# Kernel optimization log

Hardware: AMD Instinct MI355X
Metric: run time of the kernel (lower is better)

Reference implementation:

```python
import jax, jax.numpy as jnp
import numpy as np

N_NODES = 50000
N_EDGES = 400000
D = 128


def _rgg_layer(x, src, tgt, Wk, Wq, Wv, Ws, b, n_nodes):
    # Node-level projections (dense GEMMs, as in PyG which applies Linear before message passing)
    k = x @ Wk  # lin_key, gathered at targets
    q = x @ Wq  # lin_query, gathered at sources
    v = x @ Wv  # lin_value, gathered at sources
    # Per-edge gather + sigmoid gate + elementwise message
    eta = jax.nn.sigmoid(k[tgt] + q[src])  # [E, D]
    msg = eta * v[src]                      # [E, D]
    # Scatter-add aggregation to target nodes
    agg = jax.ops.segment_sum(msg, tgt, num_segments=n_nodes)
    # Root/skip connection + bias
    return agg + x @ Ws + b


def setup_inputs() -> dict:
    key = jax.random.key(0)
    ks = jax.random.split(key, 12)
    s = 1.0 / np.sqrt(D)
    x = jax.random.normal(ks[0], (N_NODES, D), dtype=jnp.float32)
    edge_index = jax.random.randint(ks[1], (2, N_EDGES), 0, N_NODES, dtype=jnp.int64)
    W = lambda k: (jax.random.normal(k, (D, D), dtype=jnp.float32) * s)
    return {
        "x": x,
        "edge_index": edge_index,
        "Wk1": W(ks[2]), "Wq1": W(ks[3]), "Wv1": W(ks[4]), "Ws1": W(ks[5]),
        "b1": jnp.zeros((D,), dtype=jnp.float32),
        "Wk2": W(ks[6]), "Wq2": W(ks[7]), "Wv2": W(ks[8]), "Ws2": W(ks[9]),
        "b2": jnp.zeros((D,), dtype=jnp.float32),
    }


def reference(x, edge_index, Wk1, Wq1, Wv1, Ws1, b1, Wk2, Wq2, Wv2, Ws2, b2):
    src, tgt = edge_index[0], edge_index[1]
    n = x.shape[0]
    h = _rgg_layer(x, src, tgt, Wk1, Wq1, Wv1, Ws1, b1, n)
    h = jax.nn.relu(h)
    # F.dropout treated as identity (deterministic/inference reference)
    out = _rgg_layer(h, src, tgt, Wk2, Wq2, Wv2, Ws2, b2, n)
    return out
```

## Files before the change

kernel.cpp:

```cpp
#include <hip/hip_runtime.h>

#define N_NODES 50000
#define D 128
#define N_EDGES 400000
#define NCHUNKS ((N_NODES + 255) / 256)
#define NBLK32 ((N_NODES + 31) / 32)
#define W_FRAG_SHORTS 16384

#define MW_BLOCKS  64
#define HIST_BLOCKS ((N_EDGES + 255) / 256)
#define PREP_BLOCKS (MW_BLOCKS + HIST_BLOCKS)

typedef short s8v  __attribute__((ext_vector_type(8)));
typedef float f4v  __attribute__((ext_vector_type(4)));

__device__ __forceinline__ unsigned int f2bf(float f) {
    unsigned int u = __float_as_uint(f);
    u += 0x7FFFu + ((u >> 16) & 1u);
    return u >> 16;
}
__device__ __forceinline__ unsigned int packbf(float a, float b) {
    return (f2bf(b) << 16) | f2bf(a);
}
__device__ __forceinline__ float bflo(unsigned int u) { return __uint_as_float(u << 16); }
__device__ __forceinline__ float bfhi(unsigned int u) { return __uint_as_float(u & 0xFFFF0000u); }
__device__ __forceinline__ float sigm(float x) {
    return __builtin_amdgcn_rcpf(1.f + __expf(-x));
}

__global__ __launch_bounds__(256)
void prep_all(const float* __restrict__ W0, const float* __restrict__ W1,
              const float* __restrict__ W2, const float* __restrict__ W3,
              const float* __restrict__ W4, const float* __restrict__ W5,
              const float* __restrict__ W6, const float* __restrict__ W7,
              short* __restrict__ Wt,
              const int* __restrict__ tgt, int* __restrict__ counts)
{
    const int b = blockIdx.x;
    if (b < MW_BLOCKS) {
        const int wsel = b >> 3;
        const float* W = (wsel == 0) ? W0 : (wsel == 1) ? W1 : (wsel == 2) ? W2 :
                         (wsel == 3) ? W3 : (wsel == 4) ? W4 : (wsel == 5) ? W5 :
                         (wsel == 6) ? W6 : W7;
        const int slot = (b & 7) * 256 + threadIdx.x;
        const int frag = slot >> 6;
        const int lane = slot & 63;
        const int n    = (frag >> 2) * 16 + (lane & 15);
        const int kc   = frag & 3;
        const int quad = lane >> 4;
        const int k0   = kc * 32 + quad * 8;
        s8v v;
#pragma unroll
        for (int j = 0; j < 8; ++j)
            v[j] = (short)f2bf(W[(size_t)(k0 + j) * D + n]);
        *(s8v*)(Wt + (size_t)wsel * W_FRAG_SHORTS + (size_t)slot * 8) = v;
    } else {
        const int e = (b - MW_BLOCKS) * 256 + threadIdx.x;
        if (e < N_EDGES) atomicAdd(&counts[tgt[e]], 1);
    }
}

__global__ __launch_bounds__(256)
void csr_scan(const int* __restrict__ counts, int* __restrict__ off,
              int* __restrict__ cursor, int* __restrict__ done_ctr,
              int* __restrict__ chunk_sum)
{
    __shared__ int s[256];
    const int b = blockIdx.x, t = threadIdx.x;
    const int i = b * 256 + t;
    const int v = (i < N_NODES) ? counts[i] : 0;
    s[t] = v;
    __syncthreads();
    for (int d = 1; d < 256; d <<= 1) {
        int tt = (t >= d) ? s[t - d] : 0;
        __syncthreads();
        s[t] += tt;
        __syncthreads();
    }
    const int incl = s[t];

    if (t == 255) {
        __hip_atomic_store(&chunk_sum[b], incl, __ATOMIC_RELAXED, __HIP_MEMORY_SCOPE_AGENT);
        __hip_atomic_fetch_add(done_ctr, 1, __ATOMIC_RELEASE, __HIP_MEMORY_SCOPE_AGENT);
    }
    if (t == 0) {
        while (__hip_atomic_load(done_ctr, __ATOMIC_ACQUIRE, __HIP_MEMORY_SCOPE_AGENT) < NCHUNKS)
            __builtin_amdgcn_s_sleep(8);
    }
    __syncthreads();

    const int pv = (t < b) ? __hip_atomic_load(&chunk_sum[t], __ATOMIC_RELAXED,
                                               __HIP_MEMORY_SCOPE_AGENT) : 0;
    __syncthreads();
    s[t] = pv;
    __syncthreads();
    for (int d = 128; d > 0; d >>= 1) {
        if (t < d) s[t] += s[t + d];
        __syncthreads();
    }
    const int base = s[0];

    if (i < N_NODES) {
        const int excl = base + incl - v;
        off[i]    = excl;
        cursor[i] = excl;
    }
    if (b == 0 && t == 0) off[N_NODES] = N_EDGES;
}

__device__ __forceinline__
void mfma_phase32(const short* As, const short* __restrict__ Wf,
                  int lane, int w, f4v acc[2][2])
{
    s8v bv[2][4];
#pragma unroll
    for (int nt2 = 0; nt2 < 2; ++nt2)
#pragma unroll
        for (int kc = 0; kc < 4; ++kc)
            bv[nt2][kc] = *(const s8v*)(Wf + (((2 * w + nt2) * 4 + kc) * 64 + lane) * 8);
#pragma unroll
    for (int mt = 0; mt < 2; ++mt)
#pragma unroll
        for (int nt2 = 0; nt2 < 2; ++nt2)
            acc[mt][nt2] = (f4v){0.f, 0.f, 0.f, 0.f};
#pragma unroll
    for (int kc = 0; kc < 4; ++kc) {
        const int sl = (lane ^ (kc << 1)) * 8;
        s8v a0 = *(const s8v*)&As[(0 * 4 + kc) * 512 + sl];
        s8v a1 = *(const s8v*)&As[(1 * 4 + kc) * 512 + sl];
#pragma unroll
        for (int nt2 = 0; nt2 < 2; ++nt2) {
            acc[0][nt2] = __builtin_amdgcn_mfma_f32_16x16x32_bf16(a0, bv[nt2][kc], acc[0][nt2], 0, 0, 0);
            acc[1][nt2] = __builtin_amdgcn_mfma_f32_16x16x32_bf16(a1, bv[nt2][kc], acc[1][nt2], 0, 0, 0);
        }
    }
}

__device__ __forceinline__
void c_to_lds32(float* Cs, int lane, int w, const f4v acc[2][2])
{
#pragma unroll
    for (int mt = 0; mt < 2; ++mt) {
        const int r0 = mt * 16 + (lane >> 4) * 4;
#pragma unroll
        for (int nt2 = 0; nt2 < 2; ++nt2) {
            const int col = w * 32 + nt2 * 16 + (lane & 15);
            const int g = col >> 2, jj = col & 3;
#pragma unroll
            for (int i = 0; i < 4; ++i) {
                const int row = r0 + i;
                const int gs  = g ^ (((row >> 2) & 3) << 2);
                Cs[row * 128 + gs * 4 + jj] = acc[mt][nt2][i];
            }
        }
    }
}

template<bool X_FP32, bool AGG_BF16>
__device__ __forceinline__
void gemm_tile(int m0, const float* __restrict__ Xf, const short* __restrict__ Xb,
               const short* __restrict__ WtL, const float* __restrict__ bias,
               short* __restrict__ Kb, unsigned int* __restrict__ QV,
               float* __restrict__ AggF, unsigned int* __restrict__ AggB,
               short* As, float* Cs, float* biasS)
{
    const int tid  = threadIdx.x;
    const int lane = tid & 63;
    const int w    = tid >> 6;

    if (tid < 128) biasS[tid] = bias[tid];

#pragma unroll
    for (int i = 0; i < 2; ++i) {
        const int m   = (tid >> 4) + 16 * i;
        const int oct = tid & 15;
        const int row = m0 + m;
        s8v v = (s8v){0, 0, 0, 0, 0, 0, 0, 0};
        if (row < N_NODES) {
            if (X_FP32) {
                const float* p = Xf + (size_t)row * D + oct * 8;
                float4 a0 = *(const float4*)p;
                float4 a1 = *(const float4*)(p + 4);
                v[0] = (short)f2bf(a0.x); v[1] = (short)f2bf(a0.y);
                v[2] = (short)f2bf(a0.z); v[3] = (short)f2bf(a0.w);
                v[4] = (short)f2bf(a1.x); v[5] = (short)f2bf(a1.y);
                v[6] = (short)f2bf(a1.z); v[7] = (short)f2bf(a1.w);
            } else {
                v = *(const s8v*)(Xb + (size_t)row * D + oct * 8);
            }
        }
        const int kc = oct >> 2, quad = oct & 3;
        const int frag = (m >> 4) * 4 + kc;
        const int slot = ((m & 15) + 16 * quad) ^ (kc << 1);
        *(s8v*)&As[frag * 512 + slot * 8] = v;
    }

    f4v acc[2][2], accV[2][2];
    __syncthreads();

    mfma_phase32(As, WtL + 0 * W_FRAG_SHORTS, lane, w, acc);
    c_to_lds32(Cs, lane, w, acc);
    __syncthreads();
#pragma unroll
    for (int j = 0; j < 4; ++j) {
        const int c   = tid + 256 * j;
        const int row = c >> 5, gg = c & 31;
        const int gs  = gg ^ (((row >> 2) & 3) << 2);
        const f4v vv  = *(const f4v*)&Cs[row * 128 + gs * 4];
        const int grow = m0 + row;
        if (grow < N_NODES) {
            uint2* kp = (uint2*)((unsigned int*)Kb + (size_t)grow * 64 + gg * 2);
            *kp = make_uint2(packbf(vv[0], vv[1]), packbf(vv[2], vv[3]));
        }
    }
    __syncthreads();

    mfma_phase32(As, WtL + 1 * W_FRAG_SHORTS, lane, w, acc);
    mfma_phase32(As, WtL + 2 * W_FRAG_SHORTS, lane, w, accV);
    c_to_lds32(Cs, lane, w, acc);
    __syncthreads();
    unsigned int qp0[4], qp1[4];
#pragma unroll
    for (int j = 0; j < 4; ++j) {
        const int c   = tid + 256 * j;
        const int row = c >> 5, gg = c & 31;
        const int gs  = gg ^ (((row >> 2) & 3) << 2);
        const f4v vv  = *(const f4v*)&Cs[row * 128 + gs * 4];
        qp0[j] = packbf(vv[0], vv[1]);
        qp1[j] = packbf(vv[2], vv[3]);
    }
    __syncthreads();
    c_to_lds32(Cs, lane, w, accV);
    __syncthreads();
#pragma unroll
    for (int j = 0; j < 4; ++j) {
        const int c   = tid + 256 * j;
        const int row = c >> 5, gg = c & 31;
        const int gs  = gg ^ (((row >> 2) & 3) << 2);
        const f4v vv  = *(const f4v*)&Cs[row * 128 + gs * 4];
        const int grow = m0 + row;
        if (grow < N_NODES) {
            uint4* qvp = (uint4*)(QV + (size_t)grow * 128 + gg * 4);
            *qvp = make_uint4(qp0[j], packbf(vv[0], vv[1]),
                              qp1[j], packbf(vv[2], vv[3]));
        }
    }
    __syncthreads();

    mfma_phase32(As, WtL + 3 * W_FRAG_SHORTS, lane, w, acc);
    c_to_lds32(Cs, lane, w, acc);
    __syncthreads();
#pragma unroll
    for (int j = 0; j < 4; ++j) {
        const int c   = tid + 256 * j;
        const int row = c >> 5, gg = c & 31;
        const int gs  = gg ^ (((row >> 2) & 3) << 2);
        const f4v vv  = *(const f4v*)&Cs[row * 128 + gs * 4];
        const int grow = m0 + row;
        if (grow >= N_NODES) continue;
        const float4 bv = *(const float4*)&biasS[gg * 4];
        const float o0 = vv[0] + bv.x, o1 = vv[1] + bv.y;
        const float o2 = vv[2] + bv.z, o3 = vv[3] + bv.w;
        if (AGG_BF16) {
            uint2* ap = (uint2*)(AggB + (size_t)grow * 64 + gg * 2);
            *ap = make_uint2(packbf(o0, o1), packbf(o2, o3));
        } else {
            *(float4*)&AggF[(size_t)grow * D + gg * 4] = make_float4(o0, o1, o2, o3);
        }
    }
}

__global__ __launch_bounds__(256, 4)
void gemm1_scatter(const float* __restrict__ X, const short* __restrict__ WtL,
                   const float* __restrict__ bias,
                   short* __restrict__ Kb, unsigned int* __restrict__ QV,
                   unsigned int* __restrict__ AggB,
                   const int* __restrict__ src, const int* __restrict__ tgt,
                   int* __restrict__ cursor, int* __restrict__ es)
{
    __shared__ __align__(16) short As[4096];
    __shared__ __align__(16) float Cs[4096];
    __shared__ __align__(16) float biasS[128];

    if (blockIdx.x < NBLK32) {
        gemm_tile<true, true>(blockIdx.x * 32, X, nullptr, WtL, bias,
                              Kb, QV, nullptr, AggB, As, Cs, biasS);
    } else {
        const int e = (blockIdx.x - NBLK32) * 256 + threadIdx.x;
        if (e < N_EDGES) {
            int pos = atomicAdd(&cursor[tgt[e]], 1);
            es[pos] = src[e];
        }
    }
}

__global__ __launch_bounds__(256, 4)
void gemm2(const short* __restrict__ Hb, const short* __restrict__ WtL,
           const float* __restrict__ bias,
           short* __restrict__ Kb, unsigned int* __restrict__ QV,
           float* __restrict__ AggF)
{
    __shared__ __align__(16) short As[4096];
    __shared__ __align__(16) float Cs[4096];
    __shared__ __align__(16) float biasS[128];
    gemm_tile<false, false>(blockIdx.x * 32, nullptr, Hb, WtL, bias,
                            Kb, QV, AggF, nullptr, As, Cs, biasS);
}

template<bool FIRST>
__global__ __launch_bounds__(256)
void node_agg(const int* __restrict__ off, const int* __restrict__ es,
              const short* __restrict__ K, const unsigned int* __restrict__ QV,
              const void* __restrict__ Skip, float* __restrict__ OutF,
              unsigned int* __restrict__ Hb)
{
    const int lane = threadIdx.x & 63;
    const int t    = __builtin_amdgcn_readfirstlane(blockIdx.x * 4 + (threadIdx.x >> 6));

    const unsigned int ku = ((const unsigned int*)K)[(size_t)t * 64 + lane];
    const float kx = bflo(ku), ky = bfhi(ku);

    float skx, sky;
    if (FIRST) {
        const unsigned int su = ((const unsigned int*)Skip)[(size_t)t * 64 + lane];
        skx = bflo(su); sky = bfhi(su);
    } else {
        const float2 s2 = ((const float2*)Skip)[(size_t)t * 64 + lane];
        skx = s2.x; sky = s2.y;
    }

    float ax = 0.f, ay = 0.f, bx = 0.f, by = 0.f;
    const int e0 = __builtin_amdgcn_readfirstlane(off[t]);
    const int e1 = __builtin_amdgcn_readfirstlane(off[t + 1]);

    int e = e0;
    for (; e + 8 <= e1; e += 8) {
        const int sv = es[e + (lane & 7)];
        uint2 g[8];
#pragma unroll
        for (int u = 0; u < 8; ++u) {
            const int s = __builtin_amdgcn_readlane(sv, u);
            g[u] = ((const uint2*)(QV + (size_t)s * 128))[lane];
        }
#pragma unroll
        for (int u = 0; u < 8; ++u) {
            if (u & 1) {
                bx += bflo(g[u].y) * sigm(kx + bflo(g[u].x));
                by += bfhi(g[u].y) * sigm(ky + bfhi(g[u].x));
            } else {
                ax += bflo(g[u].y) * sigm(kx + bflo(g[u].x));
                ay += bfhi(g[u].y) * sigm(ky + bfhi(g[u].x));
            }
        }
    }
    if (e + 4 <= e1) {
        const int sv = es[e + (lane & 3)];
        uint2 g[4];
#pragma unroll
        for (int u = 0; u < 4; ++u) {
            const int s = __builtin_amdgcn_readlane(sv, u);
            g[u] = ((const uint2*)(QV + (size_t)s * 128))[lane];
        }
#pragma unroll
        for (int u = 0; u < 4; ++u) {
            if (u & 1) {
                bx += bflo(g[u].y) * sigm(kx + bflo(g[u].x));
                by += bfhi(g[u].y) * sigm(ky + bfhi(g[u].x));
            } else {
                ax += bflo(g[u].y) * sigm(kx + bflo(g[u].x));
                ay += bfhi(g[u].y) * sigm(ky + bfhi(g[u].x));
            }
        }
        e += 4;
    }
    for (; e < e1; ++e) {
        const int s0 = __builtin_amdgcn_readfirstlane(es[e]);
        const uint2 g0 = ((const uint2*)(QV + (size_t)s0 * 128))[lane];
        ax += bflo(g0.y) * sigm(kx + bflo(g0.x));
        ay += bfhi(g0.y) * sigm(ky + bfhi(g0.x));
    }

    const float rx = skx + ax + bx;
    const float ry = sky + ay + by;

    if (FIRST) {
        Hb[(size_t)t * 64 + lane] = packbf(fmaxf(rx, 0.f), fmaxf(ry, 0.f));
    } else {
        ((float2*)OutF)[(size_t)t * 64 + lane] = make_float2(rx, ry);
    }
}

extern "C" void kernel_launch(void* const* d_in, const int* in_sizes, int n_in,
                              void* d_out, int out_size, void* d_ws, size_t ws_size,
                              hipStream_t stream)
{
    const float* x   = (const float*)d_in[0];
    const int*   ei  = (const int*)d_in[1];
    const float* Wk1 = (const float*)d_in[2];
    const float* Wq1 = (const float*)d_in[3];
    const float* Wv1 = (const float*)d_in[4];
    const float* Ws1 = (const float*)d_in[5];
    const float* b1  = (const float*)d_in[6];
    const float* Wk2 = (const float*)d_in[7];
    const float* Wq2 = (const float*)d_in[8];
    const float* Wv2 = (const float*)d_in[9];
    const float* Ws2 = (const float*)d_in[10];
    const float* b2  = (const float*)d_in[11];

    const int* src = ei;
    const int* tgt = ei + N_EDGES;

    const size_t nd = (size_t)N_NODES * D;
    short* kb   = (short*)d_ws;
    short* qv   = kb + nd;
    short* hb   = qv + 2 * nd;
    short* ag1  = hb + nd;
    short* wt   = ag1 + nd;
    int* counts    = (int*)(wt + 8 * W_FRAG_SHORTS);
    int* done_ctr  = counts + N_NODES;
    int* off       = counts + N_NODES + 2;
    int* cursor    = off + N_NODES + 1;
    int* es        = cursor + N_NODES;
    int* chunk_sum = es + N_EDGES;
    float* out = (float*)d_out;

    hipMemsetAsync(counts, 0, (N_NODES + 2) * sizeof(int), stream);
    prep_all<<<PREP_BLOCKS, 256, 0, stream>>>(Wk1, Wq1, Wv1, Ws1, Wk2, Wq2, Wv2, Ws2,
                                              wt, tgt, counts);
    csr_scan<<<NCHUNKS, 256, 0, stream>>>(counts, off, cursor, done_ctr, chunk_sum);

    gemm1_scatter<<<NBLK32 + HIST_BLOCKS, 256, 0, stream>>>(
        x, wt, b1, kb, (unsigned int*)qv, (unsigned int*)ag1, src, tgt, cursor, es);
    node_agg<true><<<N_NODES / 4, 256, 0, stream>>>(off, es, kb, (const unsigned int*)qv,
                                                    ag1, nullptr, (unsigned int*)hb);

    gemm2<<<NBLK32, 256, 0, stream>>>(hb, wt + 4 * W_FRAG_SHORTS, b2,
                                      kb, (unsigned int*)qv, out);
    node_agg<false><<<N_NODES / 4, 256, 0, stream>>>(off, es, kb, (const unsigned int*)qv,
                                                     out, out, nullptr);
}
```

Before: 256.5 us.

## Use 64-row GEMM tiles and write MFMA results directly via DPP lane swaps

Each GEMM block now covers 64 node rows instead of 32, so every weight fragment loaded from global memory feeds four row tiles instead of two. The LDS staging buffer for the output tile and its many barriers are gone. Accumulators are instead paired across neighbouring lanes with a DPP swap, then packed to bf16 and stored straight to global memory. Launch bounds drop to 3 blocks per SM to allow for the larger register footprint, which lowers occupancy and makes the direct stores less coalesced than the old row-contiguous LDS-staged writes.

```diff
diff --git a/kernel.cpp b/kernel.cpp
--- a/kernel.cpp
+++ b/kernel.cpp
@@ -4,7 +4,7 @@
 #define D 128
 #define N_EDGES 400000
 #define NCHUNKS ((N_NODES + 255) / 256)
-#define NBLK32 ((N_NODES + 31) / 32)
+#define NBLK64 ((N_NODES + 63) / 64)
 #define W_FRAG_SHORTS 16384
 
 #define MW_BLOCKS  64
@@ -26,6 +26,29 @@
 __device__ __forceinline__ float bfhi(unsigned int u) { return __uint_as_float(u & 0xFFFF0000u); }
 __device__ __forceinline__ float sigm(float x) {
     return __builtin_amdgcn_rcpf(1.f + __expf(-x));
+}
+__device__ __forceinline__ float xor1(float x) {
+    return __uint_as_float((unsigned int)__builtin_amdgcn_mov_dpp(
+        (int)__float_as_uint(x), 0xB1, 0xF, 0xF, true));
+}
+__device__ __forceinline__ void pair_vals(const f4v a, int odd,
+                                          float& loA, float& hiA,
+                                          float& loB, float& hiB)
+{
+    const float e0 = xor1(a[0]), e1 = xor1(a[1]);
+    const float e2 = xor1(a[2]), e3 = xor1(a[3]);
+    loA = odd ? e2 : a[0];
+    hiA = odd ? a[2] : e0;
+    loB = odd ? e3 : a[1];
+    hiB = odd ? a[3] : e1;
+}
+__device__ __forceinline__ void pack_pairs(const f4v a, int odd,
+                                           unsigned int& wA, unsigned int& wB)
+{
+    float loA, hiA, loB, hiB;
+    pair_vals(a, odd, loA, hiA, loB, hiB);
+    wA = packbf(loA, hiA);
+    wB = packbf(loB, hiB);
 }
 
 __global__ __launch_bounds__(256)
@@ -109,8 +132,8 @@
 }
 
 __device__ __forceinline__
-void mfma_phase32(const short* As, const short* __restrict__ Wf,
-                  int lane, int w, f4v acc[2][2])
+void mfma_phase64(const short* As, const short* __restrict__ Wf,
+                  int lane, int w, f4v acc[4][2])
 {
     s8v bv[2][4];
 #pragma unroll
@@ -119,39 +142,18 @@
         for (int kc = 0; kc < 4; ++kc)
             bv[nt2][kc] = *(const s8v*)(Wf + (((2 * w + nt2) * 4 + kc) * 64 + lane) * 8);
 #pragma unroll
-    for (int mt = 0; mt < 2; ++mt)
+    for (int mt = 0; mt < 4; ++mt)
 #pragma unroll
         for (int nt2 = 0; nt2 < 2; ++nt2)
             acc[mt][nt2] = (f4v){0.f, 0.f, 0.f, 0.f};
 #pragma unroll
     for (int kc = 0; kc < 4; ++kc) {
         const int sl = (lane ^ (kc << 1)) * 8;
-        s8v a0 = *(const s8v*)&As[(0 * 4 + kc) * 512 + sl];
-        s8v a1 = *(const s8v*)&As[(1 * 4 + kc) * 512 + sl];
-#pragma unroll
-        for (int nt2 = 0; nt2 < 2; ++nt2) {
-            acc[0][nt2] = __builtin_amdgcn_mfma_f32_16x16x32_bf16(a0, bv[nt2][kc], acc[0][nt2], 0, 0, 0);
-            acc[1][nt2] = __builtin_amdgcn_mfma_f32_16x16x32_bf16(a1, bv[nt2][kc], acc[1][nt2], 0, 0, 0);
-        }
-    }
-}
-
-__device__ __forceinline__
-void c_to_lds32(float* Cs, int lane, int w, const f4v acc[2][2])
-{
-#pragma unroll
-    for (int mt = 0; mt < 2; ++mt) {
-        const int r0 = mt * 16 + (lane >> 4) * 4;
-#pragma unroll
-        for (int nt2 = 0; nt2 < 2; ++nt2) {
-            const int col = w * 32 + nt2 * 16 + (lane & 15);
-            const int g = col >> 2, jj = col & 3;
-#pragma unroll
-            for (int i = 0; i < 4; ++i) {
-                const int row = r0 + i;
-                const int gs  = g ^ (((row >> 2) & 3) << 2);
-                Cs[row * 128 + gs * 4 + jj] = acc[mt][nt2][i];
-            }
+#pragma unroll
+        for (int mt = 0; mt < 4; ++mt) {
+            s8v a = *(const s8v*)&As[(mt * 4 + kc) * 512 + sl];
+            acc[mt][0] = __builtin_amdgcn_mfma_f32_16x16x32_bf16(a, bv[0][kc], acc[mt][0], 0, 0, 0);
+            acc[mt][1] = __builtin_amdgcn_mfma_f32_16x16x32_bf16(a, bv[1][kc], acc[mt][1], 0, 0, 0);
         }
     }
 }
@@ -160,9 +162,9 @@
 __device__ __forceinline__
 void gemm_tile(int m0, const float* __restrict__ Xf, const short* __restrict__ Xb,
                const short* __restrict__ WtL, const float* __restrict__ bias,
-               short* __restrict__ Kb, unsigned int* __restrict__ QV,
+               unsigned int* __restrict__ Kw, unsigned int* __restrict__ QV,
                float* __restrict__ AggF, unsigned int* __restrict__ AggB,
-               short* As, float* Cs, float* biasS)
+               short* As, float* biasS)
 {
     const int tid  = threadIdx.x;
     const int lane = tid & 63;
@@ -171,7 +173,7 @@
     if (tid < 128) biasS[tid] = bias[tid];
 
 #pragma unroll
-    for (int i = 0; i < 2; ++i) {
+    for (int i = 0; i < 4; ++i) {
         const int m   = (tid >> 4) + 16 * i;
         const int oct = tid & 15;
         const int row = m0 + m;
@@ -194,83 +196,82 @@
         const int slot = ((m & 15) + 16 * quad) ^ (kc << 1);
         *(s8v*)&As[frag * 512 + slot * 8] = v;
     }
-
-    f4v acc[2][2], accV[2][2];
     __syncthreads();
 
-    mfma_phase32(As, WtL + 0 * W_FRAG_SHORTS, lane, w, acc);
-    c_to_lds32(Cs, lane, w, acc);
-    __syncthreads();
-#pragma unroll
-    for (int j = 0; j < 4; ++j) {
-        const int c   = tid + 256 * j;
-        const int row = c >> 5, gg = c & 31;
-        const int gs  = gg ^ (((row >> 2) & 3) << 2);
-        const f4v vv  = *(const f4v*)&Cs[row * 128 + gs * 4];
-        const int grow = m0 + row;
-        if (grow < N_NODES) {
-            uint2* kp = (uint2*)((unsigned int*)Kb + (size_t)grow * 64 + gg * 2);
-            *kp = make_uint2(packbf(vv[0], vv[1]), packbf(vv[2], vv[3]));
-        }
-    }
-    __syncthreads();
-
-    mfma_phase32(As, WtL + 1 * W_FRAG_SHORTS, lane, w, acc);
-    mfma_phase32(As, WtL + 2 * W_FRAG_SHORTS, lane, w, accV);
-    c_to_lds32(Cs, lane, w, acc);
-    __syncthreads();
-    unsigned int qp0[4], qp1[4];
-#pragma unroll
-    for (int j = 0; j < 4; ++j) {
-        const int c   = tid + 256 * j;
-        const int row = c >> 5, gg = c & 31;
-        const int gs  = gg ^ (((row >> 2) & 3) << 2);
-        const f4v vv  = *(const f4v*)&Cs[row * 128 + gs * 4];
-        qp0[j] = packbf(vv[0], vv[1]);
-        qp1[j] = packbf(vv[2], vv[3]);
-    }
-    __syncthreads();
-    c_to_lds32(Cs, lane, w, accV);
-    __syncthreads();
-#pragma unroll
-    for (int j = 0; j < 4; ++j) {
-        const int c   = tid + 256 * j;
-        const int row = c >> 5, gg = c & 31;
-        const int gs  = gg ^ (((row >> 2) & 3) << 2);
-        const f4v vv  = *(const f4v*)&Cs[row * 128 + gs * 4];
-        const int grow = m0 + row;
-        if (grow < N_NODES) {
-            uint4* qvp = (uint4*)(QV + (size_t)grow * 128 + gg * 4);
-            *qvp = make_uint4(qp0[j], packbf(vv[0], vv[1]),
-                              qp1[j], packbf(vv[2], vv[3]));
-        }
-    }
-    __syncthreads();
-
-    mfma_phase32(As, WtL + 3 * W_FRAG_SHORTS, lane, w, acc);
-    c_to_lds32(Cs, lane, w, acc);
-    __syncthreads();
-#pragma unroll
-    for (int j = 0; j < 4; ++j) {
-        const int c   = tid + 256 * j;
-        const int row = c >> 5, gg = c & 31;
-        const int gs  = gg ^ (((row >> 2) & 3) << 2);
-        const f4v vv  = *(const f4v*)&Cs[row * 128 + gs * 4];
-        const int grow = m0 + row;
-        if (grow >= N_NODES) continue;
-        const float4 bv = *(const float4*)&biasS[gg * 4];
-        const float o0 = vv[0] + bv.x, o1 = vv[1] + bv.y;
-        const float o2 = vv[2] + bv.z, o3 = vv[3] + bv.w;
-        if (AGG_BF16) {
-            uint2* ap = (uint2*)(AggB + (size_t)grow * 64 + gg * 2);
-            *ap = make_uint2(packbf(o0, o1), packbf(o2, o3));
-        } else {
-            *(float4*)&AggF[(size_t)grow * D + gg * 4] = make_float4(o0, o1, o2, o3);
-        }
-    }
-}
-
-__global__ __launch_bounds__(256, 4)
+    const int odd  = lane & 1;
+    const int qrow = (lane >> 4) * 4;
+    const int cp   = (lane & 15) >> 1;
+
+    f4v acc[4][2], accV[4][2];
+
+    mfma_phase64(As, WtL + 0 * W_FRAG_SHORTS, lane, w, acc);
+#pragma unroll
+    for (int mt = 0; mt < 4; ++mt) {
+        const int rA = m0 + mt * 16 + qrow + odd * 2;
+#pragma unroll
+        for (int nt2 = 0; nt2 < 2; ++nt2) {
+            unsigned int wA, wB;
+            pack_pairs(acc[mt][nt2], odd, wA, wB);
+            const int wcol = w * 16 + nt2 * 8 + cp;
+            if (rA < N_NODES)     Kw[(size_t)rA * 64 + wcol]       = wA;
+            if (rA + 1 < N_NODES) Kw[(size_t)(rA + 1) * 64 + wcol] = wB;
+        }
+    }
+
+    mfma_phase64(As, WtL + 1 * W_FRAG_SHORTS, lane, w, acc);
+    mfma_phase64(As, WtL + 2 * W_FRAG_SHORTS, lane, w, accV);
+#pragma unroll
+    for (int mt = 0; mt < 4; ++mt) {
+        const int rA = m0 + mt * 16 + qrow + odd * 2;
+#pragma unroll
+        for (int nt2 = 0; nt2 < 2; ++nt2) {
+            unsigned int qA, qB, vA, vB;
+            pack_pairs(acc[mt][nt2],  odd, qA, qB);
+            pack_pairs(accV[mt][nt2], odd, vA, vB);
+            const int wcol = w * 16 + nt2 * 8 + cp;
+            if (rA < N_NODES)
+                *(uint2*)&QV[(size_t)rA * 128 + wcol * 2]       = make_uint2(qA, vA);
+            if (rA + 1 < N_NODES)
+                *(uint2*)&QV[(size_t)(rA + 1) * 128 + wcol * 2] = make_uint2(qB, vB);
+        }
+    }
+
+    mfma_phase64(As, WtL + 3 * W_FRAG_SHORTS, lane, w, acc);
+    if (AGG_BF16) {
+#pragma unroll
+        for (int mt = 0; mt < 4; ++mt) {
+            const int rA = m0 + mt * 16 + qrow + odd * 2;
+#pragma unroll
+            for (int nt2 = 0; nt2 < 2; ++nt2) {
+                float loA, hiA, loB, hiB;
+                pair_vals(acc[mt][nt2], odd, loA, hiA, loB, hiB);
+                const int wcol = w * 16 + nt2 * 8 + cp;
+                const float2 bp = *(const float2*)&biasS[2 * wcol];
+                if (rA < N_NODES)
+                    AggB[(size_t)rA * 64 + wcol]       = packbf(loA + bp.x, hiA + bp.y);
+                if (rA + 1 < N_NODES)
+                    AggB[(size_t)(rA + 1) * 64 + wcol] = packbf(loB + bp.x, hiB + bp.y);
+            }
+        }
+    } else {
+#pragma unroll
+        for (int mt = 0; mt < 4; ++mt) {
+            const int r0g = m0 + mt * 16 + qrow;
+#pragma unroll
+            for (int nt2 = 0; nt2 < 2; ++nt2) {
+                const int col = w * 32 + nt2 * 16 + (lane & 15);
+                const float b = biasS[col];
+#pragma unroll
+                for (int i = 0; i < 4; ++i) {
+                    if (r0g + i < N_NODES)
+                        AggF[(size_t)(r0g + i) * D + col] = acc[mt][nt2][i] + b;
+                }
+            }
+        }
+    }
+}
+
+__global__ __launch_bounds__(256, 3)
 void gemm1_scatter(const float* __restrict__ X, const short* __restrict__ WtL,
                    const float* __restrict__ bias,
                    short* __restrict__ Kb, unsigned int* __restrict__ QV,
@@ -278,15 +279,14 @@
                    const int* __restrict__ src, const int* __restrict__ tgt,
                    int* __restrict__ cursor, int* __restrict__ es)
 {
-    __shared__ __align__(16) short As[4096];
-    __shared__ __align__(16) float Cs[4096];
+    __shared__ __align__(16) short As[8192];
     __shared__ __align__(16) float biasS[128];
 
-    if (blockIdx.x < NBLK32) {
-        gemm_tile<true, true>(blockIdx.x * 32, X, nullptr, WtL, bias,
-                              Kb, QV, nullptr, AggB, As, Cs, biasS);
+    if (blockIdx.x < NBLK64) {
+        gemm_tile<true, true>(blockIdx.x * 64, X, nullptr, WtL, bias,
+                              (unsigned int*)Kb, QV, nullptr, AggB, As, biasS);
     } else {
-        const int e = (blockIdx.x - NBLK32) * 256 + threadIdx.x;
+        const int e = (blockIdx.x - NBLK64) * 256 + threadIdx.x;
         if (e < N_EDGES) {
             int pos = atomicAdd(&cursor[tgt[e]], 1);
             es[pos] = src[e];
@@ -294,17 +294,16 @@
     }
 }
 
-__global__ __launch_bounds__(256, 4)
+__global__ __launch_bounds__(256, 3)
 void gemm2(const short* __restrict__ Hb, const short* __restrict__ WtL,
            const float* __restrict__ bias,
            short* __restrict__ Kb, unsigned int* __restrict__ QV,
            float* __restrict__ AggF)
 {
-    __shared__ __align__(16) short As[4096];
-    __shared__ __align__(16) float Cs[4096];
+    __shared__ __align__(16) short As[8192];
     __shared__ __align__(16) float biasS[128];
-    gemm_tile<false, false>(blockIdx.x * 32, nullptr, Hb, WtL, bias,
-                            Kb, QV, AggF, nullptr, As, Cs, biasS);
+    gemm_tile<false, false>(blockIdx.x * 64, nullptr, Hb, WtL, bias,
+                            (unsigned int*)Kb, QV, AggF, nullptr, As, biasS);
 }
 
 template<bool FIRST>
@@ -429,12 +428,12 @@
                                               wt, tgt, counts);
     csr_scan<<<NCHUNKS, 256, 0, stream>>>(counts, off, cursor, done_ctr, chunk_sum);
 
-    gemm1_scatter<<<NBLK32 + HIST_BLOCKS, 256, 0, stream>>>(
+    gemm1_scatter<<<NBLK64 + HIST_BLOCKS, 256, 0, stream>>>(
         x, wt, b1, kb, (unsigned int*)qv, (unsigned int*)ag1, src, tgt, cursor, es);
     node_agg<true><<<N_NODES / 4, 256, 0, stream>>>(off, es, kb, (const unsigned int*)qv,
                                                     ag1, nullptr, (unsigned int*)hb);
 
-    gemm2<<<NBLK32, 256, 0, stream>>>(hb, wt + 4 * W_FRAG_SHORTS, b2,
+    gemm2<<<NBLK64, 256, 0, stream>>>(hb, wt + 4 * W_FRAG_SHORTS, b2,
                                       kb, (unsigned int*)qv, out);
     node_agg<false><<<N_NODES / 4, 256, 0, stream>>>(off, es, kb, (const unsigned int*)qv,
                                                      out, out, nullptr);
```

After: 273.2 us. +6.5%, slower.

## Use per-wave LDS transpose in GEMM epilogue, removing block barriers

Applied to the files above, without the earlier changes.

The GEMM epilogue now transposes each wave's 32x32 accumulator slice through a private LDS region and writes whole row segments per lane, in place of a block-wide Cs staging buffer with several __syncthreads per projection. B fragments are loaded separately from the MFMA call, launch bounds rise to 5 waves per EU, and the scatter blocks are placed before the GEMM blocks in the fused launch so the atomics start earlier. Each lane now holds 16 floats of row output and issues wider stores, which adds register pressure and changes the LDS access pattern.

```diff
diff --git a/kernel.cpp b/kernel.cpp
--- a/kernel.cpp
+++ b/kernel.cpp
@@ -109,15 +109,18 @@
 }
 
 __device__ __forceinline__
-void mfma_phase32(const short* As, const short* __restrict__ Wf,
-                  int lane, int w, f4v acc[2][2])
-{
-    s8v bv[2][4];
+void load_b32(const short* __restrict__ Wf, int lane, int w, s8v bv[2][4])
+{
 #pragma unroll
     for (int nt2 = 0; nt2 < 2; ++nt2)
 #pragma unroll
         for (int kc = 0; kc < 4; ++kc)
             bv[nt2][kc] = *(const s8v*)(Wf + (((2 * w + nt2) * 4 + kc) * 64 + lane) * 8);
+}
+
+__device__ __forceinline__
+void mfma32(const short* As, const s8v bv[2][4], int lane, f4v acc[2][2])
+{
 #pragma unroll
     for (int mt = 0; mt < 2; ++mt)
 #pragma unroll
@@ -137,22 +140,23 @@
 }
 
 __device__ __forceinline__
-void c_to_lds32(float* Cs, int lane, int w, const f4v acc[2][2])
-{
-#pragma unroll
-    for (int mt = 0; mt < 2; ++mt) {
-        const int r0 = mt * 16 + (lane >> 4) * 4;
+void frag_rows(float* CsW, int lane, const f4v acc[2][2], float out[16])
+{
+    const int cl = lane & 15, rb = lane >> 4, x7 = lane & 7;
+#pragma unroll
+    for (int mt = 0; mt < 2; ++mt)
 #pragma unroll
         for (int nt2 = 0; nt2 < 2; ++nt2) {
-            const int col = w * 32 + nt2 * 16 + (lane & 15);
-            const int g = col >> 2, jj = col & 3;
-#pragma unroll
-            for (int i = 0; i < 4; ++i) {
-                const int row = r0 + i;
-                const int gs  = g ^ (((row >> 2) & 3) << 2);
-                Cs[row * 128 + gs * 4 + jj] = acc[mt][nt2][i];
-            }
-        }
+            const int lc = nt2 * 16 + cl;
+            const int u  = lc * 8 + ((mt * 4 + rb) ^ x7);
+            *(f4v*)&CsW[u * 4] = acc[mt][nt2];
+        }
+    const int lr = lane >> 1, ch = lane & 1;
+#pragma unroll
+    for (int j = 0; j < 16; ++j) {
+        const int lc = ch * 16 + j;
+        const int u  = lc * 8 + ((lr >> 2) ^ (lc & 7));
+        out[j] = CsW[u * 4 + (lr & 3)];
     }
 }
 
@@ -160,7 +164,7 @@
 __device__ __forceinline__
 void gemm_tile(int m0, const float* __restrict__ Xf, const short* __restrict__ Xb,
                const short* __restrict__ WtL, const float* __restrict__ bias,
-               short* __restrict__ Kb, unsigned int* __restrict__ QV,
+               unsigned int* __restrict__ Kw, unsigned int* __restrict__ QV,
                float* __restrict__ AggF, unsigned int* __restrict__ AggB,
                short* As, float* Cs, float* biasS)
 {
@@ -194,86 +198,76 @@
         const int slot = ((m & 15) + 16 * quad) ^ (kc << 1);
         *(s8v*)&As[frag * 512 + slot * 8] = v;
     }
-
-    f4v acc[2][2], accV[2][2];
     __syncthreads();
 
-    mfma_phase32(As, WtL + 0 * W_FRAG_SHORTS, lane, w, acc);
-    c_to_lds32(Cs, lane, w, acc);
-    __syncthreads();
-#pragma unroll
-    for (int j = 0; j < 4; ++j) {
-        const int c   = tid + 256 * j;
-        const int row = c >> 5, gg = c & 31;
-        const int gs  = gg ^ (((row >> 2) & 3) << 2);
-        const f4v vv  = *(const f4v*)&Cs[row * 128 + gs * 4];
-        const int grow = m0 + row;
-        if (grow < N_NODES) {
-            uint2* kp = (uint2*)((unsigned int*)Kb + (size_t)grow * 64 + gg * 2);
-            *kp = make_uint2(packbf(vv[0], vv[1]), packbf(vv[2], vv[3]));
-        }
-    }
-    __syncthreads();
-
-    mfma_phase32(As, WtL + 1 * W_FRAG_SHORTS, lane, w, acc);
-    mfma_phase32(As, WtL + 2 * W_FRAG_SHORTS, lane, w, accV);
-    c_to_lds32(Cs, lane, w, acc);
-    __syncthreads();
-    unsigned int qp0[4], qp1[4];
-#pragma unroll
-    for (int j = 0; j < 4; ++j) {
-        const int c   = tid + 256 * j;
-        const int row = c >> 5, gg = c & 31;
-        const int gs  = gg ^ (((row >> 2) & 3) << 2);
-        const f4v vv  = *(const f4v*)&Cs[row * 128 + gs * 4];
-        qp0[j] = packbf(vv[0], vv[1]);
-        qp1[j] = packbf(vv[2], vv[3]);
-    }
-    __syncthreads();
-    c_to_lds32(Cs, lane, w, accV);
-    __syncthreads();
-#pragma unroll
-    for (int j = 0; j < 4; ++j) {
-        const int c   = tid + 256 * j;
-        const int row = c >> 5, gg = c & 31;
-        const int gs  = gg ^ (((row >> 2) & 3) << 2);
-        const f4v vv  = *(const f4v*)&Cs[row * 128 + gs * 4];
-        const int grow = m0 + row;
-        if (grow < N_NODES) {
-            uint4* qvp = (uint4*)(QV + (size_t)grow * 128 + gg * 4);
-            *qvp = make_uint4(qp0[j], packbf(vv[0], vv[1]),
-                              qp1[j], packbf(vv[2], vv[3]));
-        }
-    }
-    __syncthreads();
-
-    mfma_phase32(As, WtL + 3 * W_FRAG_SHORTS, lane, w, acc);
-    c_to_lds32(Cs, lane, w, acc);
-    __syncthreads();
-#pragma unroll
-    for (int j = 0; j < 4; ++j) {
-        const int c   = tid + 256 * j;
-        const int row = c >> 5, gg = c & 31;
-        const int gs  = gg ^ (((row >> 2) & 3) << 2);
-        const f4v vv  = *(const f4v*)&Cs[row * 128 + gs * 4];
-        const int grow = m0 + row;
-        if (grow >= N_NODES) continue;
-        const float4 bv = *(const float4*)&biasS[gg * 4];
-        const float o0 = vv[0] + bv.x, o1 = vv[1] + bv.y;
-        const float o2 = vv[2] + bv.z, o3 = vv[3] + bv.w;
+    float* CsW = Cs + w * 1024;
+    const int lr   = lane >> 1;
+    const int ch   = lane & 1;
+    const int grow = m0 + lr;
+    const bool rok = grow < N_NODES;
+
+    f4v acc[2][2];
+    s8v bv[2][4];
+    float ro[16];
+
+    load_b32(WtL + 0 * W_FRAG_SHORTS, lane, w, bv);
+    mfma32(As, bv, lane, acc);
+    frag_rows(CsW, lane, acc, ro);
+    if (rok) {
+        unsigned int kp[8];
+#pragma unroll
+        for (int i = 0; i < 8; ++i) kp[i] = packbf(ro[2 * i], ro[2 * i + 1]);
+        unsigned int* kb = Kw + (size_t)grow * 64 + w * 16 + ch * 8;
+        *(uint4*)kb       = make_uint4(kp[0], kp[1], kp[2], kp[3]);
+        *(uint4*)(kb + 4) = make_uint4(kp[4], kp[5], kp[6], kp[7]);
+    }
+
+    load_b32(WtL + 1 * W_FRAG_SHORTS, lane, w, bv);
+    mfma32(As, bv, lane, acc);
+    frag_rows(CsW, lane, acc, ro);
+    unsigned int qp[8];
+#pragma unroll
+    for (int i = 0; i < 8; ++i) qp[i] = packbf(ro[2 * i], ro[2 * i + 1]);
+
+    load_b32(WtL + 2 * W_FRAG_SHORTS, lane, w, bv);
+    mfma32(As, bv, lane, acc);
+    frag_rows(CsW, lane, acc, ro);
+    if (rok) {
+        unsigned int* qb = QV + (size_t)grow * 128 + (w * 16 + ch * 8) * 2;
+#pragma unroll
+        for (int i = 0; i < 8; i += 2) {
+            *(uint4*)(qb + 2 * i) = make_uint4(qp[i],     packbf(ro[2 * i],     ro[2 * i + 1]),
+                                               qp[i + 1], packbf(ro[2 * i + 2], ro[2 * i + 3]));
+        }
+    }
+
+    load_b32(WtL + 3 * W_FRAG_SHORTS, lane, w, bv);
+    mfma32(As, bv, lane, acc);
+    frag_rows(CsW, lane, acc, ro);
+#pragma unroll
+    for (int j = 0; j < 16; ++j) ro[j] += biasS[w * 32 + ch * 16 + j];
+    if (rok) {
         if (AGG_BF16) {
-            uint2* ap = (uint2*)(AggB + (size_t)grow * 64 + gg * 2);
-            *ap = make_uint2(packbf(o0, o1), packbf(o2, o3));
+            unsigned int ap[8];
+#pragma unroll
+            for (int i = 0; i < 8; ++i) ap[i] = packbf(ro[2 * i], ro[2 * i + 1]);
+            unsigned int* ab = AggB + (size_t)grow * 64 + w * 16 + ch * 8;
+            *(uint4*)ab       = make_uint4(ap[0], ap[1], ap[2], ap[3]);
+            *(uint4*)(ab + 4) = make_uint4(ap[4], ap[5], ap[6], ap[7]);
         } else {
-            *(float4*)&AggF[(size_t)grow * D + gg * 4] = make_float4(o0, o1, o2, o3);
-        }
-    }
-}
-
-__global__ __launch_bounds__(256, 4)
+            float* ob = AggF + (size_t)grow * D + w * 32 + ch * 16;
+#pragma unroll
+            for (int q = 0; q < 4; ++q)
+                *(float4*)(ob + 4 * q) = make_float4(ro[4 * q], ro[4 * q + 1],
+                                                     ro[4 * q + 2], ro[4 * q + 3]);
+        }
+    }
+}
+
+__global__ __launch_bounds__(256, 5)
 void gemm1_scatter(const float* __restrict__ X, const short* __restrict__ WtL,
                    const float* __restrict__ bias,
-                   short* __restrict__ Kb, unsigned int* __restrict__ QV,
+                   unsigned int* __restrict__ Kw, unsigned int* __restrict__ QV,
                    unsigned int* __restrict__ AggB,
                    const int* __restrict__ src, const int* __restrict__ tgt,
                    int* __restrict__ cursor, int* __restrict__ es)
@@ -282,11 +276,11 @@
     __shared__ __align__(16) float Cs[4096];
     __shared__ __align__(16) float biasS[128];
 
-    if (blockIdx.x < NBLK32) {
-        gemm_tile<true, true>(blockIdx.x * 32, X, nullptr, WtL, bias,
-                              Kb, QV, nullptr, AggB, As, Cs, biasS);
+    if (blockIdx.x >= HIST_BLOCKS) {
+        gemm_tile<true, true>((blockIdx.x - HIST_BLOCKS) * 32, X, nullptr, WtL, bias,
+                              Kw, QV, nullptr, AggB, As, Cs, biasS);
     } else {
-        const int e = (blockIdx.x - NBLK32) * 256 + threadIdx.x;
+        const int e = blockIdx.x * 256 + threadIdx.x;
         if (e < N_EDGES) {
             int pos = atomicAdd(&cursor[tgt[e]], 1);
             es[pos] = src[e];
@@ -294,17 +288,17 @@
     }
 }
 
-__global__ __launch_bounds__(256, 4)
+__global__ __launch_bounds__(256, 5)
 void gemm2(const short* __restrict__ Hb, const short* __restrict__ WtL,
            const float* __restrict__ bias,
-           short* __restrict__ Kb, unsigned int* __restrict__ QV,
+           unsigned int* __restrict__ Kw, unsigned int* __restrict__ QV,
            float* __restrict__ AggF)
 {
     __shared__ __align__(16) short As[4096];
     __shared__ __align__(16) float Cs[4096];
     __shared__ __align__(16) float biasS[128];
     gemm_tile<false, false>(blockIdx.x * 32, nullptr, Hb, WtL, bias,
-                            Kb, QV, AggF, nullptr, As, Cs, biasS);
+                            Kw, QV, AggF, nullptr, As, Cs, biasS);
 }
 
 template<bool FIRST>
@@ -430,12 +424,13 @@
     csr_scan<<<NCHUNKS, 256, 0, stream>>>(counts, off, cursor, done_ctr, chunk_sum);
 
     gemm1_scatter<<<NBLK32 + HIST_BLOCKS, 256, 0, stream>>>(
-        x, wt, b1, kb, (unsigned int*)qv, (unsigned int*)ag1, src, tgt, cursor, es);
+        x, wt, b1, (unsigned int*)kb, (unsigned int*)qv, (unsigned int*)ag1,
+        src, tgt, cursor, es);
     node_agg<true><<<N_NODES / 4, 256, 0, stream>>>(off, es, kb, (const unsigned int*)qv,
                                                     ag1, nullptr, (unsigned int*)hb);
 
     gemm2<<<NBLK32, 256, 0, stream>>>(hb, wt + 4 * W_FRAG_SHORTS, b2,
-                                      kb, (unsigned int*)qv, out);
+                                      (unsigned int*)kb, (unsigned int*)qv, out);
     node_agg<false><<<N_NODES / 4, 256, 0, stream>>>(off, es, kb, (const unsigned int*)qv,
                                                      out, out, nullptr);
 }
```

New measurement: 269.9 us. +5.2%, slower.
